# Kernel optimization log

Hardware: AMD Instinct MI355X
Metric: run time of the kernel (lower is better)

The kernel has to match this reference:

```python
import jax, jax.numpy as jnp
import numpy as np

NUM_ROUTING = 3

def _squash(s):
    # squared_norm * s / ((1 + squared_norm) * sqrt(squared_norm)), norm over last dim
    sn = jnp.sum(s * s, axis=-1, keepdims=True)
    return sn * s / ((1.0 + sn) * jnp.sqrt(sn))

def setup_inputs() -> dict:
    key = jax.random.key(0)
    kx, kw = jax.random.split(key)
    B, IN_CAPS, IN_DIM, OUT_CAPS, OUT_DIM = 64, 8192, 8, 8, 16
    x = jax.random.normal(kx, (B, IN_CAPS, IN_DIM), dtype=jnp.float32)
    W = 0.01 * jax.random.normal(kw, (IN_CAPS, OUT_CAPS, IN_DIM, OUT_DIM), dtype=jnp.float32)
    return {"x": x, "W": W}

def reference(x, W):
    # x: [B, in_caps, in_dim]; W: [in_caps, out_caps, in_dim, out_dim]
    u_hat = jnp.einsum('ijnm,bin->bijm', W, x)          # [B, i, j, m]
    temp_u_hat = jax.lax.stop_gradient(u_hat)           # detach, routing uses no grads
    B, I, J = x.shape[0], W.shape[0], W.shape[1]
    b = jnp.zeros((B, I, J), dtype=x.dtype)
    for _ in range(NUM_ROUTING - 1):
        c = jax.nn.softmax(b, axis=2)                   # over out_caps j
        s = jnp.einsum('bij,bijm->bjm', c, temp_u_hat)  # [B, j, m]
        v = _squash(s)
        b = b + jnp.einsum('bjm,bijm->bij', v, temp_u_hat)  # agreement
    c = jax.nn.softmax(b, axis=2)
    s = jnp.einsum('bij,bijm->bjm', c, u_hat)
    return _squash(s)                                   # [B, out_caps, out_dim]
```

## Files before the change

kernel.cpp:

```cpp
#include <hip/hip_runtime.h>


#define BB      64
#define ICAPS   8192
#define NDIM    8
#define JCAPS   8
#define MDIM    16
#define NBLK    256
#define ICHUNK  (ICAPS / NBLK)
#define IG      8
#define NSTAGE  (ICHUNK / IG)
#define WJ_STRIDE (NDIM * MDIM + 4)
#define WI_STRIDE (JCAPS * WJ_STRIDE)
#define S_ELEMS  (BB * JCAPS * MDIM)

template <int MODE>
__global__ __launch_bounds__(1024, 4) void caps_pass_kernel(
    const float* __restrict__ x, const float* __restrict__ W,
    const float* __restrict__ vsum, float* __restrict__ partial)
{
    __shared__ float Wlds[IG * WI_STRIDE];

    const int tid  = threadIdx.x;
    const int j    = tid & 7;
    const int b    = (tid >> 3) & 63;
    const int isub = tid >> 9;
    const int blk  = blockIdx.x;
    const int i0   = blk * ICHUNK;

    float s[MDIM];
    #pragma unroll
    for (int m = 0; m < MDIM; ++m) s[m] = 0.f;

    float v[MDIM];
    if (MODE == 1) {
        #pragma unroll
        for (int q = 0; q < 4; ++q) {
            const float4 a = *(const float4*)&vsum[(b * JCAPS + j) * MDIM + q * 4];
            v[q * 4 + 0] = a.x; v[q * 4 + 1] = a.y;
            v[q * 4 + 2] = a.z; v[q * 4 + 3] = a.w;
        }
    }

    for (int st = 0; st < NSTAGE; ++st) {
        {
            const int iL  = tid >> 7;
            const int rem = tid & 127;
            const float4* src = (const float4*)(W + (size_t)(i0 + st * IG + iL) * 1024
                                                  + rem * 8);
            float4* dst = (float4*)&Wlds[iL * WI_STRIDE + (rem >> 4) * WJ_STRIDE
                                         + (rem & 15) * 8];
            dst[0] = src[0]; dst[1] = src[1];
        }
        __syncthreads();

        #pragma unroll
        for (int t = 0; t < IG / 2; ++t) {
            const int ii = t * 2 + isub;
            const int i  = i0 + st * IG + ii;
            const float4 xa = *(const float4*)&x[((size_t)b * ICAPS + i) * NDIM];
            const float4 xb = *(const float4*)&x[((size_t)b * ICAPS + i) * NDIM + 4];
            const float xs[8] = {xa.x, xa.y, xa.z, xa.w, xb.x, xb.y, xb.z, xb.w};

            float u[MDIM];
            #pragma unroll
            for (int m = 0; m < MDIM; ++m) u[m] = 0.f;
            const float* wb = &Wlds[ii * WI_STRIDE + j * WJ_STRIDE];
            #pragma unroll
            for (int n = 0; n < NDIM; ++n) {
                const float4 w0 = *(const float4*)&wb[n * MDIM + 0];
                const float4 w1 = *(const float4*)&wb[n * MDIM + 4];
                const float4 w2 = *(const float4*)&wb[n * MDIM + 8];
                const float4 w3 = *(const float4*)&wb[n * MDIM + 12];
                const float xn = xs[n];
                u[0]  += xn * w0.x; u[1]  += xn * w0.y; u[2]  += xn * w0.z; u[3]  += xn * w0.w;
                u[4]  += xn * w1.x; u[5]  += xn * w1.y; u[6]  += xn * w1.z; u[7]  += xn * w1.w;
                u[8]  += xn * w2.x; u[9]  += xn * w2.y; u[10] += xn * w2.z; u[11] += xn * w2.w;
                u[12] += xn * w3.x; u[13] += xn * w3.y; u[14] += xn * w3.z; u[15] += xn * w3.w;
            }

            if (MODE == 0) {
                #pragma unroll
                for (int m = 0; m < MDIM; ++m) s[m] += u[m];
            } else {
                float la = v[0] * u[0],  lb = v[1] * u[1];
                float lc = v[2] * u[2],  ld = v[3] * u[3];
                la += v[4]  * u[4];  lb += v[5]  * u[5];
                lc += v[6]  * u[6];  ld += v[7]  * u[7];
                la += v[8]  * u[8];  lb += v[9]  * u[9];
                lc += v[10] * u[10]; ld += v[11] * u[11];
                la += v[12] * u[12]; lb += v[13] * u[13];
                lc += v[14] * u[14]; ld += v[15] * u[15];
                const float lp = (la + lb) + (lc + ld);
                const float e = __expf(lp);
                float d = e;
                d += __shfl_xor(d, 1);
                d += __shfl_xor(d, 2);
                d += __shfl_xor(d, 4);
                const float c = e * __builtin_amdgcn_rcpf(d);
                #pragma unroll
                for (int m = 0; m < MDIM; ++m) s[m] += c * u[m];
            }
        }
        __syncthreads();
    }

    float* red = Wlds;
    if (isub == 1) {
        #pragma unroll
        for (int q = 0; q < 4; ++q) {
            float4 o;
            o.x = s[q * 4 + 0]; o.y = s[q * 4 + 1];
            o.z = s[q * 4 + 2]; o.w = s[q * 4 + 3];
            *(float4*)&red[(b * JCAPS + j) * MDIM + q * 4] = o;
        }
    }
    __syncthreads();
    if (isub == 0) {
        const float sc = (MODE == 0) ? 0.125f : 1.0f;
        float* pp = partial + (size_t)blk * S_ELEMS + (b * JCAPS + j) * MDIM;
        #pragma unroll
        for (int q = 0; q < 4; ++q) {
            const float4 r = *(const float4*)&red[(b * JCAPS + j) * MDIM + q * 4];
            float4 o;
            o.x = (s[q * 4 + 0] + r.x) * sc; o.y = (s[q * 4 + 1] + r.y) * sc;
            o.z = (s[q * 4 + 2] + r.z) * sc; o.w = (s[q * 4 + 3] + r.w) * sc;
            *(float4*)&pp[q * 4] = o;
        }
    }
}

template <int OP>
__global__ __launch_bounds__(256) void caps_reduce_kernel(
    const float* __restrict__ partial, float* __restrict__ vsum, float* __restrict__ out)
{
    __shared__ float sd[256];
    const int bo  = blockIdx.x;
    const int tid = threadIdx.x;
    const int kg  = tid >> 6;
    const int tl  = tid & 63;
    const int t   = bo * 64 + tl;

    float a0 = 0.f, a1 = 0.f, a2 = 0.f, a3 = 0.f;
    const float* p = partial + (size_t)kg * 64 * S_ELEMS + t;
    #pragma unroll
    for (int k = 0; k < 64; k += 4) {
        a0 += p[(size_t)(k + 0) * S_ELEMS];
        a1 += p[(size_t)(k + 1) * S_ELEMS];
        a2 += p[(size_t)(k + 2) * S_ELEMS];
        a3 += p[(size_t)(k + 3) * S_ELEMS];
    }
    sd[tid] = (a0 + a1) + (a2 + a3);
    __syncthreads();

    if (tid < 64) {
        const float s = (sd[tid] + sd[64 + tid]) + (sd[128 + tid] + sd[192 + tid]);
        float sn = s * s;
        sn += __shfl_xor(sn, 1);
        sn += __shfl_xor(sn, 2);
        sn += __shfl_xor(sn, 4);
        sn += __shfl_xor(sn, 8);
        const float v = s * sqrtf(sn) / (1.f + sn);
        const int tt = bo * 64 + tid;
        if (OP == 2)      out[tt]   = v;
        else if (OP == 1) vsum[tt] += v;
        else              vsum[tt]  = v;
    }
}

extern "C" void kernel_launch(void* const* d_in, const int* in_sizes, int n_in,
                              void* d_out, int out_size, void* d_ws, size_t ws_size,
                              hipStream_t stream)
{
    const float* x = (const float*)d_in[0];
    const float* W = (const float*)d_in[1];
    float* out = (float*)d_out;

    float* partial = (float*)d_ws;
    float* vsum    = partial + (size_t)NBLK * S_ELEMS;

    caps_pass_kernel<0><<<NBLK, 1024, 0, stream>>>(x, W, vsum, partial);
    caps_reduce_kernel<0><<<128, 256, 0, stream>>>(partial, vsum, nullptr);
    caps_pass_kernel<1><<<NBLK, 1024, 0, stream>>>(x, W, vsum, partial);
    caps_reduce_kernel<1><<<128, 256, 0, stream>>>(partial, vsum, nullptr);
    caps_pass_kernel<1><<<NBLK, 1024, 0, stream>>>(x, W, vsum, partial);
    caps_reduce_kernel<2><<<128, 256, 0, stream>>>(partial, vsum, out);
}
```

Measured before the change: 192.2 us.

## Remap threads to m-quarter by batch-strided tiles to reuse W LDS loads

Each thread now handles one quarter of the out_dim for four batch rows instead of all 16 out_dim for one batch row. A single float4 W read from LDS is reused across four batch rows, which cuts LDS traffic per FMA by four. The price is four times more x loads per thread (each x element is now read by four lanes) and extra cross-lane shuffles for the agreement dot product and the softmax. The launch bound is also changed to an explicit waves-per-EU attribute.

```diff
diff --git a/kernel.cpp b/kernel.cpp
--- a/kernel.cpp
+++ b/kernel.cpp
@@ -15,30 +15,35 @@
 #define S_ELEMS  (BB * JCAPS * MDIM)
 
 template <int MODE>
-__global__ __launch_bounds__(1024, 4) void caps_pass_kernel(
+__global__ __launch_bounds__(1024)
+__attribute__((amdgpu_waves_per_eu(4, 4)))
+void caps_pass_kernel(
     const float* __restrict__ x, const float* __restrict__ W,
     const float* __restrict__ vsum, float* __restrict__ partial)
 {
     __shared__ float Wlds[IG * WI_STRIDE];
 
     const int tid  = threadIdx.x;
-    const int j    = tid & 7;
-    const int b    = (tid >> 3) & 63;
+    const int mq   = tid & 3;
+    const int j    = (tid >> 2) & 7;
+    const int bq   = (tid >> 5) & 15;
     const int isub = tid >> 9;
     const int blk  = blockIdx.x;
     const int i0   = blk * ICHUNK;
 
-    float s[MDIM];
+    float s[4][4];
     #pragma unroll
-    for (int m = 0; m < MDIM; ++m) s[m] = 0.f;
-
-    float v[MDIM];
+    for (int k = 0; k < 4; ++k)
+        #pragma unroll
+        for (int m = 0; m < 4; ++m) s[k][m] = 0.f;
+
+    float v[4][4];
     if (MODE == 1) {
         #pragma unroll
-        for (int q = 0; q < 4; ++q) {
-            const float4 a = *(const float4*)&vsum[(b * JCAPS + j) * MDIM + q * 4];
-            v[q * 4 + 0] = a.x; v[q * 4 + 1] = a.y;
-            v[q * 4 + 2] = a.z; v[q * 4 + 3] = a.w;
+        for (int k = 0; k < 4; ++k) {
+            const float4 a = *(const float4*)
+                &vsum[((bq + 16 * k) * JCAPS + j) * MDIM + mq * 4];
+            v[k][0] = a.x; v[k][1] = a.y; v[k][2] = a.z; v[k][3] = a.w;
         }
     }
 
@@ -58,48 +63,64 @@
         for (int t = 0; t < IG / 2; ++t) {
             const int ii = t * 2 + isub;
             const int i  = i0 + st * IG + ii;
-            const float4 xa = *(const float4*)&x[((size_t)b * ICAPS + i) * NDIM];
-            const float4 xb = *(const float4*)&x[((size_t)b * ICAPS + i) * NDIM + 4];
-            const float xs[8] = {xa.x, xa.y, xa.z, xa.w, xb.x, xb.y, xb.z, xb.w};
-
-            float u[MDIM];
+
+            float xs[4][8];
             #pragma unroll
-            for (int m = 0; m < MDIM; ++m) u[m] = 0.f;
-            const float* wb = &Wlds[ii * WI_STRIDE + j * WJ_STRIDE];
+            for (int k = 0; k < 4; ++k) {
+                const size_t xo = ((size_t)(bq + 16 * k) * ICAPS + i) * NDIM;
+                const float4 xa = *(const float4*)&x[xo];
+                const float4 xb = *(const float4*)&x[xo + 4];
+                xs[k][0] = xa.x; xs[k][1] = xa.y; xs[k][2] = xa.z; xs[k][3] = xa.w;
+                xs[k][4] = xb.x; xs[k][5] = xb.y; xs[k][6] = xb.z; xs[k][7] = xb.w;
+            }
+
+            float u[4][4];
+            #pragma unroll
+            for (int k = 0; k < 4; ++k)
+                #pragma unroll
+                for (int m = 0; m < 4; ++m) u[k][m] = 0.f;
+            const float* wb = &Wlds[ii * WI_STRIDE + j * WJ_STRIDE + mq * 4];
             #pragma unroll
             for (int n = 0; n < NDIM; ++n) {
-                const float4 w0 = *(const float4*)&wb[n * MDIM + 0];
-                const float4 w1 = *(const float4*)&wb[n * MDIM + 4];
-                const float4 w2 = *(const float4*)&wb[n * MDIM + 8];
-                const float4 w3 = *(const float4*)&wb[n * MDIM + 12];
-                const float xn = xs[n];
-                u[0]  += xn * w0.x; u[1]  += xn * w0.y; u[2]  += xn * w0.z; u[3]  += xn * w0.w;
-                u[4]  += xn * w1.x; u[5]  += xn * w1.y; u[6]  += xn * w1.z; u[7]  += xn * w1.w;
-                u[8]  += xn * w2.x; u[9]  += xn * w2.y; u[10] += xn * w2.z; u[11] += xn * w2.w;
-                u[12] += xn * w3.x; u[13] += xn * w3.y; u[14] += xn * w3.z; u[15] += xn * w3.w;
+                const float4 wq = *(const float4*)&wb[n * MDIM];
+                #pragma unroll
+                for (int k = 0; k < 4; ++k) {
+                    const float xn = xs[k][n];
+                    u[k][0] += xn * wq.x; u[k][1] += xn * wq.y;
+                    u[k][2] += xn * wq.z; u[k][3] += xn * wq.w;
+                }
             }
 
             if (MODE == 0) {
                 #pragma unroll
-                for (int m = 0; m < MDIM; ++m) s[m] += u[m];
+                for (int k = 0; k < 4; ++k)
+                    #pragma unroll
+                    for (int m = 0; m < 4; ++m) s[k][m] += u[k][m];
             } else {
-                float la = v[0] * u[0],  lb = v[1] * u[1];
-                float lc = v[2] * u[2],  ld = v[3] * u[3];
-                la += v[4]  * u[4];  lb += v[5]  * u[5];
-                lc += v[6]  * u[6];  ld += v[7]  * u[7];
-                la += v[8]  * u[8];  lb += v[9]  * u[9];
-                lc += v[10] * u[10]; ld += v[11] * u[11];
-                la += v[12] * u[12]; lb += v[13] * u[13];
-                lc += v[14] * u[14]; ld += v[15] * u[15];
-                const float lp = (la + lb) + (lc + ld);
-                const float e = __expf(lp);
-                float d = e;
-                d += __shfl_xor(d, 1);
-                d += __shfl_xor(d, 2);
-                d += __shfl_xor(d, 4);
-                const float c = e * __builtin_amdgcn_rcpf(d);
-                #pragma unroll
-                for (int m = 0; m < MDIM; ++m) s[m] += c * u[m];
+                float lp[4];
+                #pragma unroll
+                for (int k = 0; k < 4; ++k)
+                    lp[k] = u[k][0] * v[k][0] + u[k][1] * v[k][1]
+                          + u[k][2] * v[k][2] + u[k][3] * v[k][3];
+                #pragma unroll
+                for (int k = 0; k < 4; ++k) lp[k] += __shfl_xor(lp[k], 1);
+                #pragma unroll
+                for (int k = 0; k < 4; ++k) lp[k] += __shfl_xor(lp[k], 2);
+                float e[4], d[4];
+                #pragma unroll
+                for (int k = 0; k < 4; ++k) { e[k] = __expf(lp[k]); d[k] = e[k]; }
+                #pragma unroll
+                for (int k = 0; k < 4; ++k) d[k] += __shfl_xor(d[k], 4);
+                #pragma unroll
+                for (int k = 0; k < 4; ++k) d[k] += __shfl_xor(d[k], 8);
+                #pragma unroll
+                for (int k = 0; k < 4; ++k) d[k] += __shfl_xor(d[k], 16);
+                #pragma unroll
+                for (int k = 0; k < 4; ++k) {
+                    const float c = e[k] * __builtin_amdgcn_rcpf(d[k]);
+                    #pragma unroll
+                    for (int m = 0; m < 4; ++m) s[k][m] += c * u[k][m];
+                }
             }
         }
         __syncthreads();
@@ -108,24 +129,24 @@
     float* red = Wlds;
     if (isub == 1) {
         #pragma unroll
-        for (int q = 0; q < 4; ++q) {
+        for (int k = 0; k < 4; ++k) {
             float4 o;
-            o.x = s[q * 4 + 0]; o.y = s[q * 4 + 1];
-            o.z = s[q * 4 + 2]; o.w = s[q * 4 + 3];
-            *(float4*)&red[(b * JCAPS + j) * MDIM + q * 4] = o;
+            o.x = s[k][0]; o.y = s[k][1]; o.z = s[k][2]; o.w = s[k][3];
+            *(float4*)&red[((bq + 16 * k) * JCAPS + j) * MDIM + mq * 4] = o;
         }
     }
     __syncthreads();
     if (isub == 0) {
         const float sc = (MODE == 0) ? 0.125f : 1.0f;
-        float* pp = partial + (size_t)blk * S_ELEMS + (b * JCAPS + j) * MDIM;
-        #pragma unroll
-        for (int q = 0; q < 4; ++q) {
-            const float4 r = *(const float4*)&red[(b * JCAPS + j) * MDIM + q * 4];
+        float* pp = partial + (size_t)blk * S_ELEMS;
+        #pragma unroll
+        for (int k = 0; k < 4; ++k) {
+            const int off = ((bq + 16 * k) * JCAPS + j) * MDIM + mq * 4;
+            const float4 r = *(const float4*)&red[off];
             float4 o;
-            o.x = (s[q * 4 + 0] + r.x) * sc; o.y = (s[q * 4 + 1] + r.y) * sc;
-            o.z = (s[q * 4 + 2] + r.z) * sc; o.w = (s[q * 4 + 3] + r.w) * sc;
-            *(float4*)&pp[q * 4] = o;
+            o.x = (s[k][0] + r.x) * sc; o.y = (s[k][1] + r.y) * sc;
+            o.z = (s[k][2] + r.z) * sc; o.w = (s[k][3] + r.w) * sc;
+            *(float4*)&pp[off] = o;
         }
     }
 }
```

Result: slower. 307.4 us (+60.0%).
